# Kernel optimization log

Hardware: AMD Instinct MI355X
Metric: run time of the kernel (lower is better)

## Reference

```python
import jax, jax.numpy as jnp
import numpy as np

B, C, H, W = 4, 96, 64, 64
N_STATE, DT_RANK, K = 16, 6, 3


def _layernorm(x, g, b, eps=1e-5):
    m = jnp.mean(x, axis=-1, keepdims=True)
    v = jnp.mean((x - m) ** 2, axis=-1, keepdims=True)
    return (x - m) / jnp.sqrt(v + eps) * g + b


def _grid_sample(img, gx, gy):
    # F.grid_sample: bilinear, align_corners=True, zeros padding; gx,gy in [-1,1], [B,Ho,Wo]
    Bc, Cc, Hi, Wi = img.shape
    fx = (gx + 1.0) * 0.5 * (Wi - 1)
    fy = (gy + 1.0) * 0.5 * (Hi - 1)
    x0 = jnp.floor(fx)
    y0 = jnp.floor(fy)
    wx1 = fx - x0
    wy1 = fy - y0

    def tap(ix, iy, w):
        valid = ((ix >= 0) & (ix < Wi) & (iy >= 0) & (iy < Hi)).astype(img.dtype)
        ic = jnp.clip(ix, 0, Wi - 1).astype(jnp.int32)
        jc = jnp.clip(iy, 0, Hi - 1).astype(jnp.int32)
        v = jax.vmap(lambda im, yy, xx: im[:, yy, xx])(img, jc, ic)  # [B,C,Ho,Wo]
        return v * (w * valid)[:, None, :, :]

    return (tap(x0, y0, (1 - wx1) * (1 - wy1)) + tap(x0 + 1, y0, wx1 * (1 - wy1))
            + tap(x0, y0 + 1, (1 - wx1) * wy1) + tap(x0 + 1, y0 + 1, wx1 * wy1))


def _resize_bilinear(img, Ho, Wo):
    # torch F.interpolate(mode='bilinear', align_corners=False)
    Bc, Cc, Hi, Wi = img.shape

    def src(n_out, n_in):
        s = jnp.maximum((jnp.arange(n_out, dtype=img.dtype) + 0.5) * (n_in / n_out) - 0.5, 0.0)
        i0 = jnp.floor(s).astype(jnp.int32)
        i1 = jnp.minimum(i0 + 1, n_in - 1)
        return i0, i1, s - i0

    y0, y1, wy = src(Ho, Hi)
    x0, x1, wx = src(Wo, Wi)
    row = img[:, :, y0, :] * (1 - wy)[None, None, :, None] + img[:, :, y1, :] * wy[None, None, :, None]
    return row[:, :, :, x0] * (1 - wx) + row[:, :, :, x1] * wx


def _conv_offset(x, conv1_w, conv1_b, ca1_w, ca1_b, ca2_w, ca2_b, ln_g, ln_b, conv2_w):
    Bc, Cc = x.shape[:2]
    p = conv1_w.shape[-1] // 2
    x1 = jax.lax.conv_general_dilated(
        x, conv1_w, (1, 1), [(p, p), (p, p)],
        dimension_numbers=("NCHW", "OIHW", "NCHW"), feature_group_count=Cc
    ) + conv1_b[None, :, None, None]
    xc = jnp.mean(x, axis=(2, 3))  # adaptive_avg_pool2d -> (1,1)
    hid = jax.nn.gelu(xc @ ca1_w.T + ca1_b, approximate=False)
    ca = jax.nn.sigmoid(hid @ ca2_w.T + ca2_b)
    x1 = x1 * ca[:, :, None, None]
    xn = _layernorm(jnp.transpose(x1, (0, 2, 3, 1)), ln_g, ln_b)
    xg = jax.nn.gelu(jnp.transpose(xn, (0, 3, 1, 2)), approximate=False)
    return jnp.einsum("bchw,oc->bohw", xg, conv2_w[:, :, 0, 0])


def _deformable(x, rpe_table, conv1_w, conv1_b, ca1_w, ca1_b, ca2_w, ca2_b, ln_g, ln_b, conv2_w):
    Bc, Cc, Hc, Wc = x.shape
    L = Hc * Wc
    off = _conv_offset(x, conv1_w, conv1_b, ca1_w, ca1_b, ca2_w, ca2_b, ln_g, ln_b, conv2_w)
    offset = off[:, :2]
    de = off[:, 2]
    rng = jnp.array([1.0 / (Hc - 1.0), 1.0 / (Wc - 1.0)], off.dtype).reshape(1, 2, 1, 1)
    offset = jnp.transpose(jnp.tanh(offset) * rng, (0, 2, 3, 1))  # [B,H,W,2] (dy,dx)
    ry = (jnp.linspace(0.5, Hc - 0.5, Hc) / (Hc - 1.0)) * 2.0 - 1.0
    rx = (jnp.linspace(0.5, Wc - 0.5, Wc) / (Wc - 1.0)) * 2.0 - 1.0
    ref = jnp.stack(jnp.meshgrid(ry, rx, indexing="ij"), -1)  # [H,W,2] (y,x)
    pos = offset + ref[None]
    de_index = jnp.tanh(de).reshape(Bc, L)
    path_ref = (jnp.linspace(0.5, L - 0.5, L) / (L - 1.0)) * 2.0 - 1.0
    path_pos = de_index + path_ref[None]
    x_sampled = _grid_sample(x, pos[..., 1], pos[..., 0])
    rpe = jnp.broadcast_to(rpe_table[None], (Bc,) + rpe_table.shape)
    rpe_bias = _resize_bilinear(rpe, Hc, Wc)
    ky = (jnp.linspace(0.0, float(Hc), Hc) / (Hc - 1.0)) * 2.0 - 1.0
    kx = (jnp.linspace(0.0, float(Wc), Wc) / (Wc - 1.0)) * 2.0 - 1.0
    key_grid = jnp.stack(jnp.meshgrid(ky, kx, indexing="ij"), -1)
    disp = (key_grid[None] - pos) * 0.5
    pos_bias = _grid_sample(rpe_bias, disp[..., 1], disp[..., 0])
    xd = (x_sampled + pos_bias).reshape(Bc, Cc, L)
    indices = jnp.argsort(path_pos, axis=-1)  # topk(k=N, largest=False) == ascending argsort
    xs2 = jnp.take_along_axis(xd, indices[:, None, :], axis=2)
    return xs2, indices


def _selective_scan(u, delta, A, Bs, Cs, Dv, delta_bias):
    Bc, KD, L = u.shape
    Kk = Bs.shape[1]
    Dd = KD // Kk
    Ns = A.shape[1]
    delta = jax.nn.softplus(delta + delta_bias[None, :, None])
    dt4 = jnp.moveaxis(delta.reshape(Bc, Kk, Dd, L), 3, 0)
    u4 = jnp.moveaxis(u.reshape(Bc, Kk, Dd, L), 3, 0)
    Bt = jnp.moveaxis(Bs, 3, 0)
    Ct = jnp.moveaxis(Cs, 3, 0)
    A3 = A.reshape(Kk, Dd, Ns)

    @jax.checkpoint
    def step(h, inp):
        dt, ut, bt, ct = inp  # [B,K,D],[B,K,D],[B,K,N],[B,K,N]
        h = jnp.exp(dt[..., None] * A3) * h + (dt * ut)[..., None] * bt[:, :, None, :]
        return h, jnp.einsum("bkdn,bkn->bkd", h, ct)

    h0 = jnp.zeros((Bc, Kk, Dd, Ns), u.dtype)
    _, ys = jax.lax.scan(step, h0, (dt4, u4, Bt, Ct))
    ys = jnp.moveaxis(ys, 0, 3).reshape(Bc, KD, L)
    return ys + u * Dv[None, :, None]


def _forward(x, x_proj_weight, dt_projs_weight, dt_projs_bias, A_logs, Ds_param,
             conv1_w, conv1_b, ca1_w, ca1_b, ca2_w, ca2_b, ln_g, ln_b, conv2_w, rpe_table):
    Bc, Dd, Hc, Wc = x.shape
    L = Hc * Wc
    Kk, _, R = dt_projs_weight.shape
    Ns = A_logs.shape[1]
    xs0 = x.reshape(Bc, Dd, L)
    xs2, indices = _deformable(x, rpe_table, conv1_w, conv1_b, ca1_w, ca1_b, ca2_w, ca2_b, ln_g, ln_b, conv2_w)
    xs = jnp.stack([xs0, xs0[..., ::-1], xs2], axis=1)  # [B,3,D,L]
    x_dbl = jnp.einsum("bkdl,kcd->bkcl", xs, x_proj_weight)
    dts, Bs, Cs = jnp.split(x_dbl, [R, R + Ns], axis=2)
    dts = jnp.einsum("bkrl,kdr->bkdl", dts, dt_projs_weight)
    A = -jnp.exp(A_logs)
    ys = _selective_scan(xs.reshape(Bc, Kk * Dd, L), dts.reshape(Bc, Kk * Dd, L),
                         A, Bs, Cs, Ds_param, dt_projs_bias.reshape(-1))
    ys = ys.reshape(Bc, Kk, Dd, L)
    inv = jnp.argsort(indices, axis=-1)  # inverse permutation (DeformableLayerReverse)
    y2 = jnp.take_along_axis(ys[:, 2], inv[:, None, :], axis=2)
    y = (ys[:, 0] + ys[:, 1][..., ::-1] + y2) / 3.0
    return jnp.transpose(y, (0, 2, 1)).reshape(Bc, Hc, Wc, Dd)


def setup_inputs():
    key = jax.random.key(0)
    ks = jax.random.split(key, 12)
    f = jnp.float32
    return {
        "x": jax.random.normal(ks[0], (B, C, H, W), f),
        "x_proj_weight": jax.random.normal(ks[1], (K, DT_RANK + 2 * N_STATE, C), f) * 0.05,
        "dt_projs_weight": jax.random.normal(ks[2], (K, C, DT_RANK), f) * 0.05,
        "dt_projs_bias": jax.random.normal(ks[3], (K, C), f) * 0.1,
        "A_logs": jnp.tile(jnp.log(jnp.arange(1, N_STATE + 1, dtype=f))[None, :], (K * C, 1)),
        "Ds_param": jnp.ones((K * C,), f),
        "conv1_w": jax.random.normal(ks[4], (C, 1, 9, 9), f) * 0.05,
        "conv1_b": jnp.zeros((C,), f),
        "ca1_w": jax.random.normal(ks[5], (C // 16, C), f) * 0.1,
        "ca1_b": jnp.zeros((C // 16,), f),
        "ca2_w": jax.random.normal(ks[6], (C, C // 16), f) * 0.1,
        "ca2_b": jnp.zeros((C,), f),
        "ln_g": jnp.ones((C,), f),
        "ln_b": jnp.zeros((C,), f),
        "conv2_w": jax.random.normal(ks[7], (3, C, 1, 1), f) * 0.05,
        "rpe_table": jax.random.normal(ks[8], (C, 7, 7), f) * 0.01,
    }


def reference(x, x_proj_weight, dt_projs_weight, dt_projs_bias, A_logs, Ds_param,
              conv1_w, conv1_b, ca1_w, ca1_b, ca2_w, ca2_b, ln_g, ln_b, conv2_w, rpe_table):
    return _forward(x, x_proj_weight, dt_projs_weight, dt_projs_bias, A_logs, Ds_param,
                    conv1_w, conv1_b, ca1_w, ca1_b, ca2_w, ca2_b, ln_g, ln_b, conv2_w, rpe_table)
```

## Files before the change

### kernel.cpp

```cpp
#include <hip/hip_runtime.h>

#define BB 4
#define CC 96
#define HH 64
#define WW 64
#define LL 4096
#define KK 3
#define RR 6
#define NN 16

__device__ __forceinline__ float geluf(float x){
    return 0.5f * x * (1.0f + erff(x * 0.70710678118654752f));
}
__device__ __forceinline__ float softplusf(float x){
    return fmaxf(x, 0.0f) + log1pf(expf(-fabsf(x)));
}
__device__ __forceinline__ float sigmoidf(float x){
    return 1.0f / (1.0f + expf(-x));
}

__global__ __launch_bounds__(256) void k_meanrpe(const float* __restrict__ x, float* __restrict__ xc,
                                                 const float* __restrict__ rpet, float* __restrict__ rpe){
    int blk = blockIdx.x;
    if (blk < BB*CC){
        const float* p = x + (size_t)blk * LL;
        float s = 0.f;
        for (int i = threadIdx.x; i < LL; i += 256) s += p[i];
        __shared__ float red[256];
        red[threadIdx.x] = s; __syncthreads();
        for (int st = 128; st > 0; st >>= 1){
            if (threadIdx.x < st) red[threadIdx.x] += red[threadIdx.x + st];
            __syncthreads();
        }
        if (threadIdx.x == 0) xc[blk] = red[0] * (1.0f / LL);
    } else {
        int gid = (blk - BB*CC) * 256 + threadIdx.x;
        int l = gid & (LL-1); int c = gid >> 12;
        int h = l >> 6, w = l & 63;
        float sy = fmaxf((h + 0.5f) * (7.0f/64.0f) - 0.5f, 0.f);
        float sx = fmaxf((w + 0.5f) * (7.0f/64.0f) - 0.5f, 0.f);
        int y0 = (int)floorf(sy); int x0 = (int)floorf(sx);
        float wy = sy - (float)y0, wx = sx - (float)x0;
        int y1 = min(y0 + 1, 6), x1i = min(x0 + 1, 6);
        const float* tp = rpet + c * 49;
        float r0 = tp[y0*7 + x0] * (1.f - wy) + tp[y1*7 + x0] * wy;
        float r1 = tp[y0*7 + x1i] * (1.f - wy) + tp[y1*7 + x1i] * wy;
        rpe[gid] = r0 * (1.f - wx) + r1 * wx;
    }
}

__global__ __launch_bounds__(128) void k_ca(const float* __restrict__ xc,
                     const float* __restrict__ w1, const float* __restrict__ b1,
                     const float* __restrict__ w2, const float* __restrict__ b2,
                     float* __restrict__ ca){
    int b = blockIdx.x;
    int t = threadIdx.x;
    __shared__ float hid[CC/16];
    if (t < CC/16){
        float a = b1[t];
        for (int d = 0; d < CC; d++) a += w1[t*CC + d] * xc[b*CC + d];
        hid[t] = geluf(a);
    }
    __syncthreads();
    if (t < CC){
        float a = b2[t];
        #pragma unroll
        for (int i = 0; i < CC/16; i++) a += w2[t*(CC/16) + i] * hid[i];
        ca[b*CC + t] = sigmoidf(a);
    }
}

__global__ __launch_bounds__(256) void k_conv(const float* __restrict__ x, const float* __restrict__ w,
                       const float* __restrict__ bias, const float* __restrict__ ca,
                       float* __restrict__ x1){
    int tid4 = blockIdx.x * 256 + threadIdx.x;
    int wq4 = (tid4 & 15) * 4;
    int rest = tid4 >> 4;
    int h = rest & 63;
    int bc = rest >> 6;
    int c = bc % CC; int b = bc / CC;
    const float* xp = x + (size_t)bc * LL;
    const float* wp = w + c * 81;
    float a0 = 0.f, a1 = 0.f, a2 = 0.f, a3 = 0.f;
    #pragma unroll
    for (int ky = 0; ky < 9; ky++){
        int yy = h + ky - 4;
        if (yy < 0 || yy >= HH) continue;
        const float4* row4 = (const float4*)(xp + yy*WW);
        int g = wq4 >> 2;
        float4 q0 = (wq4 >= 4)  ? row4[g-1] : make_float4(0.f,0.f,0.f,0.f);
        float4 q1 = row4[g];
        float4 q2 = (wq4 < 60)  ? row4[g+1] : make_float4(0.f,0.f,0.f,0.f);
        float v[12] = {q0.x,q0.y,q0.z,q0.w, q1.x,q1.y,q1.z,q1.w, q2.x,q2.y,q2.z,q2.w};
        const float* wr = wp + ky*9;
        #pragma unroll
        for (int kx = 0; kx < 9; kx++){
            float wk = wr[kx];
            a0 = fmaf(v[kx],   wk, a0);
            a1 = fmaf(v[kx+1], wk, a1);
            a2 = fmaf(v[kx+2], wk, a2);
            a3 = fmaf(v[kx+3], wk, a3);
        }
    }
    float sc = ca[b*CC + c];
    float bb = bias[c];
    float4 o = make_float4((a0+bb)*sc, (a1+bb)*sc, (a2+bb)*sc, (a3+bb)*sc);
    *(float4*)(x1 + (size_t)bc*LL + h*WW + wq4) = o;
}

__global__ __launch_bounds__(256) void k_off(const float* __restrict__ x1,
                      const float* __restrict__ g, const float* __restrict__ bta,
                      const float* __restrict__ w2,
                      float* __restrict__ posy, float* __restrict__ posx, float* __restrict__ path){
    int blk = blockIdx.x;
    int tile = blk & 127; int b = blk >> 7;
    int li = threadIdx.x & 31;
    int cg = threadIdx.x >> 5;
    int l = tile * 32 + li;
    const float* p = x1 + (size_t)b * CC * LL + l;
    float v[12];
    float s = 0.f, ss = 0.f;
    #pragma unroll
    for (int j = 0; j < 12; j++){
        float t = p[(size_t)(cg*12 + j) * LL];
        v[j] = t; s += t; ss += t*t;
    }
    __shared__ float ls[8][32], lss[8][32];
    ls[cg][li] = s; lss[cg][li] = ss;
    __syncthreads();
    s = 0.f; ss = 0.f;
    #pragma unroll
    for (int g2 = 0; g2 < 8; g2++){ s += ls[g2][li]; ss += lss[g2][li]; }
    float m = s * (1.0f/CC);
    float rstd = rsqrtf(ss*(1.0f/CC) - m*m + 1e-5f);
    float a0 = 0.f, a1 = 0.f, a2 = 0.f;
    #pragma unroll
    for (int j = 0; j < 12; j++){
        int c = cg*12 + j;
        float xn = (v[j]-m)*rstd*g[c] + bta[c];
        float xg = geluf(xn);
        a0 = fmaf(w2[c],      xg, a0);
        a1 = fmaf(w2[CC+c],   xg, a1);
        a2 = fmaf(w2[2*CC+c], xg, a2);
    }
    __shared__ float la[3][8][32];
    la[0][cg][li] = a0; la[1][cg][li] = a1; la[2][cg][li] = a2;
    __syncthreads();
    if (cg < 3){
        float a = 0.f;
        #pragma unroll
        for (int g2 = 0; g2 < 8; g2++) a += la[cg][g2][li];
        int h = l >> 6, ww = l & 63;
        if (cg == 0)      posy[b*LL + l] = tanhf(a)*(1.0f/63.0f) + ((2*h+1)*(1.0f/63.0f) - 1.0f);
        else if (cg == 1) posx[b*LL + l] = tanhf(a)*(1.0f/63.0f) + ((2*ww+1)*(1.0f/63.0f) - 1.0f);
        else              path[b*LL + l] = tanhf(a) + ((l + 0.5f)*(2.0f/4095.0f) - 1.0f);
    }
}

__device__ __forceinline__ float bilin0(const float* __restrict__ img, float gx, float gy){
    float fx = (gx + 1.f) * 31.5f;
    float fy = (gy + 1.f) * 31.5f;
    float x0f = floorf(fx), y0f = floorf(fy);
    float wx = fx - x0f, wy = fy - y0f;
    int x0 = (int)x0f, y0 = (int)y0f;
    float acc = 0.f;
    bool vx0 = (x0 >= 0) & (x0 < WW), vx1 = (x0+1 >= 0) & (x0+1 < WW);
    bool vy0 = (y0 >= 0) & (y0 < HH), vy1 = (y0+1 >= 0) & (y0+1 < HH);
    if (vy0 & vx0) acc += img[y0*WW + x0]       * (1.f-wx) * (1.f-wy);
    if (vy0 & vx1) acc += img[y0*WW + x0+1]     * wx       * (1.f-wy);
    if (vy1 & vx0) acc += img[(y0+1)*WW + x0]   * (1.f-wx) * wy;
    if (vy1 & vx1) acc += img[(y0+1)*WW + x0+1] * wx       * wy;
    return acc;
}

typedef unsigned long long u64s;
__device__ __forceinline__ u64s shflx64(u64s x, int m){
    int lo = __shfl_xor((int)(unsigned)x, m);
    int hi = __shfl_xor((int)(unsigned)(x >> 32), m);
    return ((u64s)(unsigned)hi << 32) | (unsigned)lo;
}
__device__ __forceinline__ void cex(u64s& a, u64s& b, bool up){
    u64s mn = a < b ? a : b;
    u64s mx = a < b ? b : a;
    a = up ? mn : mx;
    b = up ? mx : mn;
}
__global__ __launch_bounds__(1024) void k_sortsample(
        const float* __restrict__ path, int* __restrict__ idx, int* __restrict__ inv,
        const float* __restrict__ x, const float* __restrict__ rpe,
        const float* __restrict__ posy, const float* __restrict__ posx,
        float* __restrict__ xd){
    int blk = blockIdx.x;
    if (blk < BB){
        int b = blk;
        int t = threadIdx.x;
        __shared__ u64s lds[LL];
        u64s v[4];
        #pragma unroll
        for (int r = 0; r < 4; r++){
            int e = t*4 + r;
            unsigned u = __float_as_uint(path[b*LL + e]);
            u ^= (u >> 31) ? 0xFFFFFFFFu : 0x80000000u;
            v[r] = ((u64s)u << 32) | (unsigned)e;
        }
        for (int kk = 2; kk <= LL; kk <<= 1){
            for (int j = kk >> 1; j > 0; j >>= 1){
                if (j >= 256){
                    __syncthreads();
                    #pragma unroll
                    for (int r = 0; r < 4; r++) lds[t*4 + r] = v[r];
                    __syncthreads();
                    #pragma unroll
                    for (int r = 0; r < 4; r++){
                        int e = t*4 + r;
                        u64s pv = lds[e ^ j];
                        bool up    = ((e & kk) == 0);
                        bool lower = ((e & j) == 0);
                        u64s mn = v[r] < pv ? v[r] : pv;
                        u64s mx = v[r] < pv ? pv : v[r];
                        v[r] = (up == lower) ? mn : mx;
                    }
                } else if (j >= 4){
                    int m = j >> 2;
                    #pragma unroll
                    for (int r = 0; r < 4; r++){
                        u64s pv = shflx64(v[r], m);
                        bool up    = (((t*4 + r) & kk) == 0);
                        bool lower = ((t & m) == 0);
                        u64s mn = v[r] < pv ? v[r] : pv;
                        u64s mx = v[r] < pv ? pv : v[r];
                        v[r] = (up == lower) ? mn : mx;
                    }
                } else if (j == 2){
                    bool up = (((t*4) & kk) == 0);
                    cex(v[0], v[2], up);
                    cex(v[1], v[3], up);
                } else {
                    if (kk == 2){
                        cex(v[0], v[1], true);
                        cex(v[2], v[3], false);
                    } else {
                        bool up = (((t*4) & kk) == 0);
                        cex(v[0], v[1], up);
                        cex(v[2], v[3], up);
                    }
                }
            }
        }
        #pragma unroll
        for (int r = 0; r < 4; r++){
            int e = t*4 + r;
            int id = (int)(unsigned)(v[r] & 0xFFFFFFFFu);
            idx[b*LL + e] = id;
            inv[b*LL + id] = e;
        }
    } else {
        int gid = (blk - BB) * 1024 + threadIdx.x;
        int l = gid & (LL-1); int bc = gid >> 12;
        int b = bc / CC; int c = bc % CC;
        float gy = posy[b*LL + l], gx = posx[b*LL + l];
        float v = bilin0(x + (size_t)bc * LL, gx, gy);
        int h = l >> 6, w = l & 63;
        float ky = h * (128.0f/3969.0f) - 1.0f;
        float kx = w * (128.0f/3969.0f) - 1.0f;
        float v2 = bilin0(rpe + (size_t)c * LL, (kx - gx) * 0.5f, (ky - gy) * 0.5f);
        xd[gid] = v + v2;
    }
}

__global__ __launch_bounds__(192, 1) void k_proj(const float* __restrict__ x, const float* __restrict__ xd,
    const int* __restrict__ indices, const float* __restrict__ xpw, const float* __restrict__ dtw,
    const float* __restrict__ dtb, float* __restrict__ u2, float* __restrict__ dt,
    float* __restrict__ Bst, float* __restrict__ Cst){
    int blk = blockIdx.x;
    int ltile = blk & 63; int bk = blk >> 6;
    int k = bk % KK; int b = bk / KK;
    int lane = threadIdx.x & 63;
    int w = threadIdx.x >> 6;
    const float* __restrict__ Wk = xpw + k*38*CC;
    int l = ltile * 64 + lane;
    int srcl = (k == 0) ? l : (k == 1 ? (LL-1-l) : indices[b*LL + l]);
    const float* xp = (k == 2 ? xd : x) + (size_t)b * CC * LL + srcl;

    __shared__ float vsh[CC*64];
    #pragma unroll
    for (int j = 0; j < 32; j++){
        int d = w*32 + j;
        vsh[d*64 + lane] = xp[(size_t)d * LL];
    }
    __syncthreads();

    if (w == 0){
        float acc[RR];
        #pragma unroll
        for (int i = 0; i < RR; i++) acc[i] = 0.f;
        for (int d = 0; d < CC; d++){
            float vv = vsh[d*64 + lane];
            #pragma unroll
            for (int i = 0; i < RR; i++) acc[i] = fmaf(Wk[i*CC + d], vv, acc[i]);
        }
        const float* __restrict__ Dw = dtw + k*CC*RR;
        const float* __restrict__ Db = dtb + k*CC;
        float* dtp = dt + (size_t)bk * CC * LL + l;
        #pragma unroll 8
        for (int d = 0; d < CC; d++){
            float sdt = Db[d];
            #pragma unroll
            for (int r = 0; r < RR; r++) sdt = fmaf(acc[r], Dw[d*RR + r], sdt);
            dtp[(size_t)d * LL] = softplusf(sdt);
        }
    } else if (w == 1){
        float acc[NN];
        #pragma unroll
        for (int i = 0; i < NN; i++) acc[i] = 0.f;
        for (int d = 0; d < CC; d++){
            float vv = vsh[d*64 + lane];
            #pragma unroll
            for (int i = 0; i < NN; i++) acc[i] = fmaf(Wk[(RR + i)*CC + d], vv, acc[i]);
        }
        size_t base = ((size_t)bk * LL + l) * NN;
        #pragma unroll
        for (int q = 0; q < 4; q++){
            float4 o; o.x = acc[q*4]; o.y = acc[q*4+1]; o.z = acc[q*4+2]; o.w = acc[q*4+3];
            *(float4*)(Bst + base + q*4) = o;
        }
    } else {
        float acc[NN];
        #pragma unroll
        for (int i = 0; i < NN; i++) acc[i] = 0.f;
        for (int d = 0; d < CC; d++){
            float vv = vsh[d*64 + lane];
            #pragma unroll
            for (int i = 0; i < NN; i++) acc[i] = fmaf(Wk[(RR + NN + i)*CC + d], vv, acc[i]);
        }
        size_t base = ((size_t)bk * LL + l) * NN;
        #pragma unroll
        for (int q = 0; q < 4; q++){
            float4 o; o.x = acc[q*4]; o.y = acc[q*4+1]; o.z = acc[q*4+2]; o.w = acc[q*4+3];
            *(float4*)(Cst + base + q*4) = o;
        }
        if (k == 2){
            float* up = u2 + (size_t)b * CC * LL + l;
            #pragma unroll 8
            for (int d = 0; d < CC; d++) up[(size_t)d * LL] = vsh[d*64 + lane];
        }
    }
}

#define SEG 128
#define TL 32
#define SROW 17
#define XROW 32
template<int KIND>
__device__ __forceinline__ void scan_body(int b, int d, const float* __restrict__ usrc,
    const float* __restrict__ dt, const float* __restrict__ Bst, const float* __restrict__ Cst,
    const float* __restrict__ Alog, const float* __restrict__ Ds, float* __restrict__ ys,
    float* sA, float* sB, float* sS, float* yl){
    int bk = b * KK + KIND;
    int tid = threadIdx.x;
    int ng = tid & 3;
    int seg = tid >> 2;
    int t0 = seg * TL;
    int xsw = (seg & 7) << 2;

    const float4 A4 = *(const float4*)(Alog + (KIND*CC + d)*NN + 4*ng);
    const float L2E = 1.4426950408889634f;
    float A2[4] = { -__expf(A4.x)*L2E, -__expf(A4.y)*L2E, -__expf(A4.z)*L2E, -__expf(A4.w)*L2E };
    float Dv = Ds[KIND*CC + d];

    const float* dtp = dt + ((size_t)bk * CC + d) * LL + t0;
    const float* ub = (KIND == 1)
        ? usrc + ((size_t)b*CC + d) * LL + (LL-4-t0)
        : usrc + ((size_t)b*CC + d) * LL + t0;
    const float* Bp = Bst + ((size_t)bk * LL + t0) * NN + 4*ng;
    const float* Cp = Cst + ((size_t)bk * LL + t0) * NN + 4*ng;
    float* yp = ys + ((size_t)bk * CC + d) * LL + t0;

    float h[4] = {0.f,0.f,0.f,0.f};
    float S = 0.f;
    for (int t = 0; t < TL; t += 4){
        float4 dq = *(const float4*)(dtp + t);
        float4 uq = (KIND == 1) ? *(const float4*)(ub - t) : *(const float4*)(ub + t);
        float4 Bq[4], Cq[4];
        #pragma unroll
        for (int i = 0; i < 4; i++){
            Bq[i] = *(const float4*)(Bp + (t+i)*NN);
            Cq[i] = *(const float4*)(Cp + (t+i)*NN);
        }
        float dd[4] = {dq.x, dq.y, dq.z, dq.w};
        float uu[4];
        if (KIND == 1){ uu[0]=uq.w; uu[1]=uq.z; uu[2]=uq.y; uu[3]=uq.x; }
        else          { uu[0]=uq.x; uu[1]=uq.y; uu[2]=uq.z; uu[3]=uq.w; }
        float sv[4], pv[4];
        #pragma unroll
        for (int i = 0; i < 4; i++){
            float du = dd[i] * uu[i];
            float bb[4] = {Bq[i].x, Bq[i].y, Bq[i].z, Bq[i].w};
            float cc[4] = {Cq[i].x, Cq[i].y, Cq[i].z, Cq[i].w};
            float p = 0.f;
            #pragma unroll
            for (int j = 0; j < 4; j++){
                float a = exp2f(dd[i] * A2[j]);
                h[j] = fmaf(a, h[j], du * bb[j]);
                p = fmaf(h[j], cc[j], p);
            }
            S += dd[i];
            sv[i] = S;
            p += __shfl_xor(p, 1);
            p += __shfl_xor(p, 2);
            pv[i] = fmaf(uu[i], Dv, p);
        }
        if (ng == 0){
            int xo = seg*XROW + (t ^ xsw);
            *(float4*)(sS + xo) = make_float4(sv[0], sv[1], sv[2], sv[3]);
            *(float4*)(yl + xo) = make_float4(pv[0], pv[1], pv[2], pv[3]);
        }
    }

    #pragma unroll
    for (int j = 0; j < 4; j++){
        sA[seg*SROW + 4*ng + j] = exp2f(A2[j] * S);
        sB[seg*SROW + 4*ng + j] = h[j];
    }
    __syncthreads();
    {
        int wv = tid >> 6;
        int lane = tid & 63;
        #pragma unroll
        for (int nn = 0; nn < 2; nn++){
            int n = 2*wv + nn;
            float a1 = sA[(2*lane)*SROW + n],   b1 = sB[(2*lane)*SROW + n];
            float a2 = sA[(2*lane+1)*SROW + n], b2 = sB[(2*lane+1)*SROW + n];
            float ca = a1 * a2;
            float cb = fmaf(a2, b1, b2);
            #pragma unroll
            for (int off = 1; off < 64; off <<= 1){
                float ta = __shfl_up(ca, off);
                float tb = __shfl_up(cb, off);
                if (lane >= off){
                    cb = fmaf(ca, tb, cb);
                    ca *= ta;
                }
            }
            float cb_prev = __shfl_up(cb, 1);
            if (lane == 0) cb_prev = 0.f;
            sA[(2*lane)*SROW + n]   = cb_prev;
            sA[(2*lane+1)*SROW + n] = fmaf(a1, cb_prev, b1);
        }
    }
    __syncthreads();
    float hc[4];
    #pragma unroll
    for (int j = 0; j < 4; j++) hc[j] = sA[seg*SROW + 4*ng + j];

    for (int t = 0; t < TL; t += 4){
        int xo = seg*XROW + (t ^ xsw);
        float4 sq = *(const float4*)(sS + xo);
        float4 Cq[4];
        #pragma unroll
        for (int i = 0; i < 4; i++) Cq[i] = *(const float4*)(Cp + (t+i)*NN);
        float sv[4] = {sq.x, sq.y, sq.z, sq.w};
        float yo[4];
        #pragma unroll
        for (int i = 0; i < 4; i++){
            float cc[4] = {Cq[i].x, Cq[i].y, Cq[i].z, Cq[i].w};
            float corr = 0.f;
            #pragma unroll
            for (int j = 0; j < 4; j++){
                float P = exp2f(sv[i] * A2[j]);
                corr = fmaf(P * hc[j], cc[j], corr);
            }
            corr += __shfl_xor(corr, 1);
            corr += __shfl_xor(corr, 2);
            yo[i] = corr;
        }
        if (ng == 0){
            float4 ylq = *(const float4*)(yl + xo);
            float4 o = make_float4(ylq.x + yo[0], ylq.y + yo[1], ylq.z + yo[2], ylq.w + yo[3]);
            *(float4*)(yp + t) = o;
        }
    }
}

__global__ __launch_bounds__(512) void k_scan_all(const float* __restrict__ x, const float* __restrict__ u2,
    const float* __restrict__ dt, const float* __restrict__ Bst, const float* __restrict__ Cst,
    const float* __restrict__ Alog, const float* __restrict__ Ds, float* __restrict__ ys){
    __shared__ float sA[SEG*SROW];
    __shared__ float sB[SEG*SROW];
    __shared__ float sS[SEG*XROW];
    __shared__ float yl[SEG*XROW];
    int blk = blockIdx.x;
    int k = blk / (BB*CC);
    int r = blk % (BB*CC);
    int d = r % CC; int b = r / CC;
    if (k == 0)      scan_body<0>(b, d, x,  dt, Bst, Cst, Alog, Ds, ys, sA, sB, sS, yl);
    else if (k == 1) scan_body<1>(b, d, x,  dt, Bst, Cst, Alog, Ds, ys, sA, sB, sS, yl);
    else             scan_body<2>(b, d, u2, dt, Bst, Cst, Alog, Ds, ys, sA, sB, sS, yl);
}

__global__ __launch_bounds__(256) void k_comb(const float* __restrict__ ys, const int* __restrict__ inv,
                                              float* __restrict__ out){
    int tile = blockIdx.x & 255; int b = blockIdx.x >> 8;
    int l0 = tile * 16;
    __shared__ float t0[CC * 17];
    __shared__ int invs[16];
    if (threadIdx.x < 16) invs[threadIdx.x] = inv[b*LL + l0 + threadIdx.x];
    __syncthreads();
    const float* y0p = ys + (size_t)(b*KK + 0) * CC * LL;
    const float* y1p = ys + (size_t)(b*KK + 1) * CC * LL;
    const float* y2p = ys + (size_t)(b*KK + 2) * CC * LL;
    #pragma unroll
    for (int it = 0; it < 6; it++){
        int e = it * 256 + threadIdx.x;
        int li = e & 15; int c = e >> 4;
        int l = l0 + li;
        float v = y0p[(size_t)c*LL + l] + y1p[(size_t)c*LL + (LL-1-l)] + y2p[(size_t)c*LL + invs[li]];
        t0[c*17 + li] = v * (1.0f/3.0f);
    }
    __syncthreads();
    #pragma unroll
    for (int it = 0; it < 6; it++){
        int e = it * 256 + threadIdx.x;
        int c = e % CC; int li = e / CC;
        out[((size_t)b*LL + l0 + li) * CC + c] = t0[c*17 + li];
    }
}

extern "C" void kernel_launch(void* const* d_in, const int* in_sizes, int n_in,
                              void* d_out, int out_size, void* d_ws, size_t ws_size,
                              hipStream_t stream){
    const float* x    = (const float*)d_in[0];
    const float* xpw  = (const float*)d_in[1];
    const float* dtw  = (const float*)d_in[2];
    const float* dtb  = (const float*)d_in[3];
    const float* Alog = (const float*)d_in[4];
    const float* Ds   = (const float*)d_in[5];
    const float* c1w  = (const float*)d_in[6];
    const float* c1b  = (const float*)d_in[7];
    const float* ca1w = (const float*)d_in[8];
    const float* ca1b = (const float*)d_in[9];
    const float* ca2w = (const float*)d_in[10];
    const float* ca2b = (const float*)d_in[11];
    const float* lng  = (const float*)d_in[12];
    const float* lnb  = (const float*)d_in[13];
    const float* c2w  = (const float*)d_in[14];
    const float* rpet = (const float*)d_in[15];
    float* out = (float*)d_out;

    float* ws   = (float*)d_ws;
    float* xc   = ws;
    float* ca   = xc + 384;
    float* x1   = ca + 384;
    float* rpe  = x1 + (size_t)BB*CC*LL;
    float* posy = rpe + (size_t)CC*LL;
    float* posx = posy + (size_t)BB*LL;
    float* path = posx + (size_t)BB*LL;
    float* xd   = path + (size_t)BB*LL;
    int*   idx  = (int*)(xd + (size_t)BB*CC*LL);
    int*   inv  = idx + (size_t)BB*LL;
    float* u2   = (float*)(inv + (size_t)BB*LL);
    float* dtA  = u2 + (size_t)BB*CC*LL;
    float* Bst  = dtA + (size_t)BB*KK*CC*LL;
    float* Cst  = Bst + (size_t)BB*KK*LL*NN;
    float* ysA  = Cst + (size_t)BB*KK*LL*NN;

    k_meanrpe  <<<BB*CC + (CC*LL)/256, 256, 0, stream>>>(x, xc, rpet, rpe);
    k_ca       <<<BB, 128, 0, stream>>>(xc, ca1w, ca1b, ca2w, ca2b, ca);
    k_conv     <<<(BB*CC*LL/4)/256, 256, 0, stream>>>(x, c1w, c1b, ca, x1);
    k_off      <<<BB*128, 256, 0, stream>>>(x1, lng, lnb, c2w, posy, posx, path);
    k_sortsample<<<BB + (BB*CC*LL)/1024, 1024, 0, stream>>>(path, idx, inv, x, rpe, posy, posx, xd);
    k_proj     <<<BB*KK*64, 192, 0, stream>>>(x, xd, idx, xpw, dtw, dtb, u2, dtA, Bst, Cst);
    k_scan_all <<<KK*BB*CC, 512, 0, stream>>>(x, u2, dtA, Bst, Cst, Alog, Ds, ysA);
    k_comb     <<<BB*256, 256, 0, stream>>>(ysA, inv, out);
}
```

Measured before the change: 288.1 us.

## Fuse channel-attention MLP into conv kernel and split projection reduction across waves

Removes the separate tiny channel-attention kernel launch by having each conv block recompute the small MLP hidden layer in shared memory and the per-channel sigmoid scale inline. Doubles the projection kernel's threads to 384 so each output group is computed by two waves over half the channel dimension, combined through a shared-memory reduction, to raise parallelism in a low-occupancy kernel. This adds redundant MLP work per conv block, an extra barrier, and more shared memory in the projection kernel. The __syncthreads calls sit inside branches, but every wave reaches exactly one of them.

```diff
diff --git a/kernel.cpp b/kernel.cpp
--- a/kernel.cpp
+++ b/kernel.cpp
@@ -49,29 +49,10 @@
     }
 }
 
-__global__ __launch_bounds__(128) void k_ca(const float* __restrict__ xc,
-                     const float* __restrict__ w1, const float* __restrict__ b1,
-                     const float* __restrict__ w2, const float* __restrict__ b2,
-                     float* __restrict__ ca){
-    int b = blockIdx.x;
-    int t = threadIdx.x;
-    __shared__ float hid[CC/16];
-    if (t < CC/16){
-        float a = b1[t];
-        for (int d = 0; d < CC; d++) a += w1[t*CC + d] * xc[b*CC + d];
-        hid[t] = geluf(a);
-    }
-    __syncthreads();
-    if (t < CC){
-        float a = b2[t];
-        #pragma unroll
-        for (int i = 0; i < CC/16; i++) a += w2[t*(CC/16) + i] * hid[i];
-        ca[b*CC + t] = sigmoidf(a);
-    }
-}
-
 __global__ __launch_bounds__(256) void k_conv(const float* __restrict__ x, const float* __restrict__ w,
-                       const float* __restrict__ bias, const float* __restrict__ ca,
+                       const float* __restrict__ bias, const float* __restrict__ xc,
+                       const float* __restrict__ ca1w, const float* __restrict__ ca1b,
+                       const float* __restrict__ ca2w, const float* __restrict__ ca2b,
                        float* __restrict__ x1){
     int tid4 = blockIdx.x * 256 + threadIdx.x;
     int wq4 = (tid4 & 15) * 4;
@@ -79,9 +60,25 @@
     int h = rest & 63;
     int bc = rest >> 6;
     int c = bc % CC; int b = bc / CC;
+
+    __shared__ float hids[8];
+    if (threadIdx.x < 6){
+        float a = ca1b[threadIdx.x];
+        const float* w1p = ca1w + threadIdx.x * CC;
+        const float* xcp = xc + b * CC;
+        #pragma unroll 8
+        for (int d = 0; d < CC; d++) a = fmaf(w1p[d], xcp[d], a);
+        hids[threadIdx.x] = geluf(a);
+    }
+    __syncthreads();
+    float a2 = ca2b[c];
+    #pragma unroll
+    for (int i = 0; i < 6; i++) a2 = fmaf(ca2w[c*6 + i], hids[i], a2);
+    float sc = sigmoidf(a2);
+
     const float* xp = x + (size_t)bc * LL;
     const float* wp = w + c * 81;
-    float a0 = 0.f, a1 = 0.f, a2 = 0.f, a3 = 0.f;
+    float a0 = 0.f, a1 = 0.f, a2a = 0.f, a3 = 0.f;
     #pragma unroll
     for (int ky = 0; ky < 9; ky++){
         int yy = h + ky - 4;
@@ -96,15 +93,14 @@
         #pragma unroll
         for (int kx = 0; kx < 9; kx++){
             float wk = wr[kx];
-            a0 = fmaf(v[kx],   wk, a0);
-            a1 = fmaf(v[kx+1], wk, a1);
-            a2 = fmaf(v[kx+2], wk, a2);
-            a3 = fmaf(v[kx+3], wk, a3);
-        }
-    }
-    float sc = ca[b*CC + c];
+            a0  = fmaf(v[kx],   wk, a0);
+            a1  = fmaf(v[kx+1], wk, a1);
+            a2a = fmaf(v[kx+2], wk, a2a);
+            a3  = fmaf(v[kx+3], wk, a3);
+        }
+    }
     float bb = bias[c];
-    float4 o = make_float4((a0+bb)*sc, (a1+bb)*sc, (a2+bb)*sc, (a3+bb)*sc);
+    float4 o = make_float4((a0+bb)*sc, (a1+bb)*sc, (a2a+bb)*sc, (a3+bb)*sc);
     *(float4*)(x1 + (size_t)bc*LL + h*WW + wq4) = o;
 }
 
@@ -268,7 +264,7 @@
     }
 }
 
-__global__ __launch_bounds__(192, 1) void k_proj(const float* __restrict__ x, const float* __restrict__ xd,
+__global__ __launch_bounds__(384, 1) void k_proj(const float* __restrict__ x, const float* __restrict__ xd,
     const int* __restrict__ indices, const float* __restrict__ xpw, const float* __restrict__ dtw,
     const float* __restrict__ dtb, float* __restrict__ u2, float* __restrict__ dt,
     float* __restrict__ Bst, float* __restrict__ Cst){
@@ -277,50 +273,65 @@
     int k = bk % KK; int b = bk / KK;
     int lane = threadIdx.x & 63;
     int w = threadIdx.x >> 6;
+    int p = (w >= 3) ? (w - 3) : w;
+    int hh = (w >= 3) ? 1 : 0;
+    int d0 = hh * 48;
     const float* __restrict__ Wk = xpw + k*38*CC;
     int l = ltile * 64 + lane;
     int srcl = (k == 0) ? l : (k == 1 ? (LL-1-l) : indices[b*LL + l]);
     const float* xp = (k == 2 ? xd : x) + (size_t)b * CC * LL + srcl;
 
     __shared__ float vsh[CC*64];
-    #pragma unroll
-    for (int j = 0; j < 32; j++){
-        int d = w*32 + j;
+    __shared__ float red[2][38][64];
+    #pragma unroll
+    for (int j = 0; j < 16; j++){
+        int d = w*16 + j;
         vsh[d*64 + lane] = xp[(size_t)d * LL];
     }
     __syncthreads();
 
-    if (w == 0){
+    if (p == 0){
         float acc[RR];
         #pragma unroll
         for (int i = 0; i < RR; i++) acc[i] = 0.f;
-        for (int d = 0; d < CC; d++){
+        for (int d = d0; d < d0 + 48; d++){
             float vv = vsh[d*64 + lane];
             #pragma unroll
             for (int i = 0; i < RR; i++) acc[i] = fmaf(Wk[i*CC + d], vv, acc[i]);
         }
+        #pragma unroll
+        for (int i = 0; i < RR; i++) red[hh][i][lane] = acc[i];
+        __syncthreads();
+        #pragma unroll
+        for (int i = 0; i < RR; i++) acc[i] += red[1-hh][i][lane];
         const float* __restrict__ Dw = dtw + k*CC*RR;
         const float* __restrict__ Db = dtb + k*CC;
         float* dtp = dt + (size_t)bk * CC * LL + l;
         #pragma unroll 8
-        for (int d = 0; d < CC; d++){
+        for (int d = d0; d < d0 + 48; d++){
             float sdt = Db[d];
             #pragma unroll
             for (int r = 0; r < RR; r++) sdt = fmaf(acc[r], Dw[d*RR + r], sdt);
             dtp[(size_t)d * LL] = softplusf(sdt);
         }
-    } else if (w == 1){
+    } else if (p == 1){
         float acc[NN];
         #pragma unroll
         for (int i = 0; i < NN; i++) acc[i] = 0.f;
-        for (int d = 0; d < CC; d++){
+        for (int d = d0; d < d0 + 48; d++){
             float vv = vsh[d*64 + lane];
             #pragma unroll
             for (int i = 0; i < NN; i++) acc[i] = fmaf(Wk[(RR + i)*CC + d], vv, acc[i]);
         }
+        #pragma unroll
+        for (int i = 0; i < NN; i++) red[hh][6 + i][lane] = acc[i];
+        __syncthreads();
+        #pragma unroll
+        for (int i = 0; i < NN; i++) acc[i] += red[1-hh][6 + i][lane];
         size_t base = ((size_t)bk * LL + l) * NN;
         #pragma unroll
-        for (int q = 0; q < 4; q++){
+        for (int qq = 0; qq < 2; qq++){
+            int q = hh*2 + qq;
             float4 o; o.x = acc[q*4]; o.y = acc[q*4+1]; o.z = acc[q*4+2]; o.w = acc[q*4+3];
             *(float4*)(Bst + base + q*4) = o;
         }
@@ -328,21 +339,27 @@
         float acc[NN];
         #pragma unroll
         for (int i = 0; i < NN; i++) acc[i] = 0.f;
-        for (int d = 0; d < CC; d++){
+        for (int d = d0; d < d0 + 48; d++){
             float vv = vsh[d*64 + lane];
             #pragma unroll
             for (int i = 0; i < NN; i++) acc[i] = fmaf(Wk[(RR + NN + i)*CC + d], vv, acc[i]);
         }
+        #pragma unroll
+        for (int i = 0; i < NN; i++) red[hh][22 + i][lane] = acc[i];
+        __syncthreads();
+        #pragma unroll
+        for (int i = 0; i < NN; i++) acc[i] += red[1-hh][22 + i][lane];
         size_t base = ((size_t)bk * LL + l) * NN;
         #pragma unroll
-        for (int q = 0; q < 4; q++){
+        for (int qq = 0; qq < 2; qq++){
+            int q = hh*2 + qq;
             float4 o; o.x = acc[q*4]; o.y = acc[q*4+1]; o.z = acc[q*4+2]; o.w = acc[q*4+3];
             *(float4*)(Cst + base + q*4) = o;
         }
         if (k == 2){
             float* up = u2 + (size_t)b * CC * LL + l;
             #pragma unroll 8
-            for (int d = 0; d < CC; d++) up[(size_t)d * LL] = vsh[d*64 + lane];
+            for (int d = d0; d < d0 + 48; d++) up[(size_t)d * LL] = vsh[d*64 + lane];
         }
     }
 }
@@ -565,11 +582,11 @@
     float* ysA  = Cst + (size_t)BB*KK*LL*NN;
 
     k_meanrpe  <<<BB*CC + (CC*LL)/256, 256, 0, stream>>>(x, xc, rpet, rpe);
-    k_ca       <<<BB, 128, 0, stream>>>(xc, ca1w, ca1b, ca2w, ca2b, ca);
-    k_conv     <<<(BB*CC*LL/4)/256, 256, 0, stream>>>(x, c1w, c1b, ca, x1);
+    k_conv     <<<(BB*CC*LL/4)/256, 256, 0, stream>>>(x, c1w, c1b, xc,
+                                                      ca1w, ca1b, ca2w, ca2b, x1);
     k_off      <<<BB*128, 256, 0, stream>>>(x1, lng, lnb, c2w, posy, posx, path);
     k_sortsample<<<BB + (BB*CC*LL)/1024, 1024, 0, stream>>>(path, idx, inv, x, rpe, posy, posx, xd);
-    k_proj     <<<BB*KK*64, 192, 0, stream>>>(x, xd, idx, xpw, dtw, dtb, u2, dtA, Bst, Cst);
+    k_proj     <<<BB*KK*64, 384, 0, stream>>>(x, xd, idx, xpw, dtw, dtb, u2, dtA, Bst, Cst);
     k_scan_all <<<KK*BB*CC, 512, 0, stream>>>(x, u2, dtA, Bst, Cst, Alog, Ds, ysA);
     k_comb     <<<BB*256, 256, 0, stream>>>(ysA, inv, out);
 }
```

Measured after the change: 323.1 us (median of 2 runs). 12.1% more time.
